# Kernel optimization log

Measured on AMD Instinct MI355X. Metric: run time of the kernel, lower is better.

Reference implementation:

```python
import jax, jax.numpy as jnp
import numpy as np

NUM_FEATURES = 128
NUM_FILTERS = 128

def setup_inputs() -> dict:
    key = jax.random.key(0)
    k1, k2, k3, k4, k5 = jax.random.split(key, 5)
    B, N, F = 4, 2048, NUM_FEATURES
    x = jax.random.normal(k1, (B, N, F), dtype=jnp.float32)
    A = jax.random.normal(k2, (B, N, N), dtype=jnp.float32)
    # Conv1D(num_filters, kernel_size=1, use_bias=False) == per-node linear F -> filters
    W = jax.random.normal(k3, (F, NUM_FILTERS), dtype=jnp.float32) * (1.0 / np.sqrt(F))
    # self.a: Conv1D(1, kernel_size=1) with bias == linear filters -> 1 (shared for x_i and x_j)
    a_w = jax.random.normal(k4, (NUM_FILTERS, 1), dtype=jnp.float32) * (1.0 / np.sqrt(NUM_FILTERS))
    a_b = jax.random.normal(k5, (1,), dtype=jnp.float32) * 0.01
    bias = jnp.zeros((NUM_FILTERS,), dtype=jnp.float32)
    return {"x": x, "A": A, "W": W, "a_w": a_w, "a_b": a_b, "bias": bias}

def reference(x, A, W, a_w, a_b, bias):
    # project features: [B,N,F] @ [F,Ff] -> [B,N,Ff]
    h = jnp.einsum('bnf,fg->bng', x, W)
    # shared attention projection (x_i and x_j use the same layer): [B,N,1]
    s = jnp.einsum('bng,go->bno', h, a_w) + a_b
    # additive scores s_i + s_j^T -> [B,N,N]
    e = s + jnp.swapaxes(s, 1, 2)
    e = jnp.where(e >= 0, e, 0.2 * e)  # LeakyReLU(0.2)
    attn = jax.nn.softmax(e + A, axis=-1)
    out = jnp.einsum('bij,bjg->big', attn, h) + bias
    return out
```

## Files before the change

kernel.cpp:

```cpp
#include <hip/hip_runtime.h>
#include <hip/hip_bf16.h>
#include <stdint.h>

#define BB 4
#define NN 2048
#define FF 128

typedef __attribute__((ext_vector_type(8))) short bf16x8;
typedef __attribute__((ext_vector_type(4))) float f32x4;

__device__ inline unsigned pk_bf16(float a, float b) {
    union { float f; unsigned u; } x, y;
    x.f = a; y.f = b;
    unsigned xu = x.u + (0x7fffu + ((x.u >> 16) & 1u));
    unsigned yu = y.u + (0x7fffu + ((y.u >> 16) & 1u));
    return (xu >> 16) | (yu & 0xffff0000u);
}

#define XT_P 136
#define WT_P 136

__global__ __launch_bounds__(256) void k1_proj(
    const float* __restrict__ x, const float* __restrict__ W,
    const float* __restrict__ a_w, const float* __restrict__ a_b,
    uint16_t* __restrict__ Ht, float* __restrict__ s_out)
{
    __shared__ uint16_t xt[16 * XT_P];
    __shared__ uint16_t Wt[128 * WT_P];
    __shared__ float sredw[4 * 16];

    const int t = threadIdx.x;
    const int w = t >> 6, l = t & 63;
    const int m16 = l & 15, q = l >> 4;
    const int b = blockIdx.x >> 7;
    const int n0 = (blockIdx.x & 127) << 4;

    const int c4 = (t & 31) * 4, kh = (t >> 5) * 16;
    float4 wr0[8], wr1[8];
    #pragma unroll
    for (int kk = 0; kk < 8; ++kk) {
        const int k = kh + 2 * kk;
        wr0[kk] = *(const float4*)(W + (size_t)k * 128 + c4);
        wr1[kk] = *(const float4*)(W + (size_t)(k + 1) * 128 + c4);
    }
    {
        const int row = t >> 4, c0 = (t & 15) * 8;
        const float* xr = x + ((size_t)(b * NN + n0 + row)) * FF + c0;
        const float4 v0 = *(const float4*)xr;
        const float4 v1 = *(const float4*)(xr + 4);
        unsigned* dst = (unsigned*)(xt + row * XT_P + c0);
        dst[0] = pk_bf16(v0.x, v0.y); dst[1] = pk_bf16(v0.z, v0.w);
        dst[2] = pk_bf16(v1.x, v1.y); dst[3] = pk_bf16(v1.z, v1.w);
    }
    #pragma unroll
    for (int kk = 0; kk < 8; ++kk) {
        const int k = kh + 2 * kk;
        *(unsigned*)(Wt + (c4 + 0) * WT_P + k) = pk_bf16(wr0[kk].x, wr1[kk].x);
        *(unsigned*)(Wt + (c4 + 1) * WT_P + k) = pk_bf16(wr0[kk].y, wr1[kk].y);
        *(unsigned*)(Wt + (c4 + 2) * WT_P + k) = pk_bf16(wr0[kk].z, wr1[kk].z);
        *(unsigned*)(Wt + (c4 + 3) * WT_P + k) = pk_bf16(wr0[kk].w, wr1[kk].w);
    }
    const int g0 = (2 * w) * 16 + m16, g1 = (2 * w + 1) * 16 + m16;
    const float aw0 = a_w[g0], aw1 = a_w[g1];
    __syncthreads();

    f32x4 acc0 = {}, acc1 = {};
    bf16x8 af[4];
    #pragma unroll
    for (int dk = 0; dk < 4; ++dk)
        af[dk] = *(const bf16x8*)(xt + m16 * XT_P + dk * 32 + q * 8);
    #pragma unroll
    for (int dk = 0; dk < 4; ++dk) {
        bf16x8 b0 = *(const bf16x8*)(Wt + g0 * WT_P + dk * 32 + q * 8);
        bf16x8 b1 = *(const bf16x8*)(Wt + g1 * WT_P + dk * 32 + q * 8);
        acc0 = __builtin_amdgcn_mfma_f32_16x16x32_bf16(af[dk], b0, acc0, 0, 0, 0);
        acc1 = __builtin_amdgcn_mfma_f32_16x16x32_bf16(af[dk], b1, acc1, 0, 0, 0);
    }

    float sp[4];
    #pragma unroll
    for (int r = 0; r < 4; ++r) sp[r] = acc0[r] * aw0 + acc1[r] * aw1;
    #pragma unroll
    for (int off = 1; off < 16; off <<= 1)
        #pragma unroll
        for (int r = 0; r < 4; ++r) sp[r] += __shfl_xor(sp[r], off, 64);
    if (m16 == 0) {
        #pragma unroll
        for (int r = 0; r < 4; ++r) sredw[w * 16 + q * 4 + r] = sp[r];
    }
    {
        uint2 o0 = { pk_bf16(acc0[0], acc0[1]), pk_bf16(acc0[2], acc0[3]) };
        uint2 o1 = { pk_bf16(acc1[0], acc1[1]), pk_bf16(acc1[2], acc1[3]) };
        *(uint2*)(Ht + ((size_t)(b * 128 + g0)) * NN + n0 + q * 4) = o0;
        *(uint2*)(Ht + ((size_t)(b * 128 + g1)) * NN + n0 + q * 4) = o1;
    }
    __syncthreads();
    if (t < 16)
        s_out[b * NN + n0 + t] = sredw[t] + sredw[16 + t] + sredw[32 + t] + sredw[48 + t] + a_b[0];
}

#define JS 8
#define IRND 8

__global__ __launch_bounds__(256, 2) void k2_attn(
    const float* __restrict__ A, const uint16_t* __restrict__ Ht,
    const float* __restrict__ s, uint16_t* __restrict__ po,
    float* __restrict__ prs)
{
    __shared__ float Opw[4][16 * 132];
    __shared__ float rsw[4][16];

    const int t = threadIdx.x;
    const int w = t >> 6, l = t & 63;
    const int m16 = l & 15, q = l >> 4;

    const int bx = blockIdx.x;
    const int js = bx & 7;
    const int is = (bx >> 3) & 15;
    const int b  = bx >> 7;
    const int j0 = js * 256;
    const int ibase = is * 128;

    const float* sb = s + b * NN;
    const float* Ab = A + (size_t)b * NN * NN;
    const uint16_t* Hb = Ht + (size_t)b * FF * NN;

    const int jc0 = j0 + w * 32 + q * 8;
    const int jc1 = j0 + (w + 4) * 32 + q * 8;

    float4 sj00 = *(const float4*)(sb + jc0);
    float4 sj01 = *(const float4*)(sb + jc0 + 4);
    float4 sj10 = *(const float4*)(sb + jc1);
    float4 sj11 = *(const float4*)(sb + jc1 + 4);

    bf16x8 hf0[8], hf1[8];
    #pragma unroll
    for (int gt = 0; gt < 8; ++gt) {
        const uint16_t* hp = Hb + (size_t)(gt * 16 + m16) * NN;
        hf0[gt] = *(const bf16x8*)(hp + jc0);
        hf1[gt] = *(const bf16x8*)(hp + jc1);
    }

    const float* Ar0 = Ab + (size_t)(ibase + m16) * NN;
    const float* Ar1 = Ab + (size_t)(ibase + 16 + m16) * NN;
    float4 p000 = *(const float4*)(Ar0 + jc0);
    float4 p001 = *(const float4*)(Ar0 + jc0 + 4);
    float4 p010 = *(const float4*)(Ar0 + jc1);
    float4 p011 = *(const float4*)(Ar0 + jc1 + 4);
    float4 p100 = *(const float4*)(Ar1 + jc0);
    float4 p101 = *(const float4*)(Ar1 + jc0 + 4);
    float4 p110 = *(const float4*)(Ar1 + jc1);
    float4 p111 = *(const float4*)(Ar1 + jc1 + 4);
    float si0 = sb[ibase + m16];
    float si1 = sb[ibase + 16 + m16];

    const size_t slice = (size_t)(js * BB + b);

    #pragma unroll
    for (int r = 0; r < IRND; ++r) {
        const int i0r = ibase + r * 16;
        const int i2  = ibase + ((r + 2) & (IRND - 1)) * 16;

        const float* An = Ab + (size_t)(i2 + m16) * NN;
        float4 n00 = *(const float4*)(An + jc0);
        float4 n01 = *(const float4*)(An + jc0 + 4);
        float4 n10 = *(const float4*)(An + jc1);
        float4 n11 = *(const float4*)(An + jc1 + 4);
        const float si2 = sb[i2 + m16];

        const float svv[16] = {sj00.x,sj00.y,sj00.z,sj00.w, sj01.x,sj01.y,sj01.z,sj01.w,
                               sj10.x,sj10.y,sj10.z,sj10.w, sj11.x,sj11.y,sj11.z,sj11.w};
        const float avv[16] = {p000.x,p000.y,p000.z,p000.w, p001.x,p001.y,p001.z,p001.w,
                               p010.x,p010.y,p010.z,p010.w, p011.x,p011.y,p011.z,p011.w};
        float pv[16]; float rs = 0.f;
        #pragma unroll
        for (int j = 0; j < 16; ++j) {
            float e = si0 + svv[j];
            e = fmaxf(e, 0.2f * e);
            pv[j] = __expf(e + avv[j]);
            rs += pv[j];
        }
        union { unsigned u[4]; bf16x8 v; } fa0, fa1;
        #pragma unroll
        for (int j = 0; j < 4; ++j) {
            fa0.u[j] = pk_bf16(pv[2 * j], pv[2 * j + 1]);
            fa1.u[j] = pk_bf16(pv[8 + 2 * j], pv[9 + 2 * j]);
        }

        f32x4 acc[8];
        #pragma unroll
        for (int gt = 0; gt < 8; ++gt) {
            f32x4 z = {0.f, 0.f, 0.f, 0.f};
            z = __builtin_amdgcn_mfma_f32_16x16x32_bf16(fa0.v, hf0[gt], z, 0, 0, 0);
            acc[gt] = __builtin_amdgcn_mfma_f32_16x16x32_bf16(fa1.v, hf1[gt], z, 0, 0, 0);
        }

        rs += __shfl_xor(rs, 16, 64);
        rs += __shfl_xor(rs, 32, 64);
        if (q == 0) rsw[w][m16] = rs;

        #pragma unroll
        for (int gt = 0; gt < 8; ++gt)
            #pragma unroll
            for (int rr = 0; rr < 4; ++rr)
                Opw[w][(q * 4 + rr) * 132 + gt * 16 + m16] = acc[gt][rr];
        asm volatile("s_waitcnt lgkmcnt(0)\n\ts_barrier" ::: "memory");

        {
            const int row = t >> 4, k8 = (t & 15) * 8;
            float v[8] = {0.f,0.f,0.f,0.f,0.f,0.f,0.f,0.f};
            #pragma unroll
            for (int sl = 0; sl < 4; ++sl) {
                float4 u0 = *(const float4*)&Opw[sl][row * 132 + k8];
                float4 u1 = *(const float4*)&Opw[sl][row * 132 + k8 + 4];
                v[0] += u0.x; v[1] += u0.y; v[2] += u0.z; v[3] += u0.w;
                v[4] += u1.x; v[5] += u1.y; v[6] += u1.z; v[7] += u1.w;
            }
            unsigned* op = (unsigned*)(po + ((slice * NN + i0r + row) * FF + k8));
            op[0] = pk_bf16(v[0], v[1]); op[1] = pk_bf16(v[2], v[3]);
            op[2] = pk_bf16(v[4], v[5]); op[3] = pk_bf16(v[6], v[7]);
            if (t < 16)
                prs[slice * NN + i0r + t] = rsw[0][t] + rsw[1][t] + rsw[2][t] + rsw[3][t];
        }
        asm volatile("s_waitcnt lgkmcnt(0)\n\ts_barrier" ::: "memory");

        p000 = p100; p001 = p101; p010 = p110; p011 = p111; si0 = si1;
        p100 = n00;  p101 = n01;  p110 = n10;  p111 = n11;  si1 = si2;
    }
}

__global__ __launch_bounds__(256) void k3_red(
    const uint16_t* __restrict__ po, const float* __restrict__ prs,
    const float* __restrict__ bias, float* __restrict__ out)
{
    const int gid = blockIdx.x * 256 + threadIdx.x;
    const int g8 = (gid & 15) * 8;
    const int i = (gid >> 4) & (NN - 1);
    const int b = gid >> 15;

    float v[8] = {0.f,0.f,0.f,0.f,0.f,0.f,0.f,0.f};
    float rsum = 0.f;
    #pragma unroll
    for (int js = 0; js < JS; ++js) {
        const size_t base = (size_t)(js * BB + b) * NN + i;
        const uint4 pv_ = *(const uint4*)(po + base * FF + g8);
        const unsigned uu[4] = {pv_.x, pv_.y, pv_.z, pv_.w};
        #pragma unroll
        for (int k = 0; k < 4; ++k) {
            union { unsigned u; float f; } lo, hi;
            lo.u = uu[k] << 16;
            hi.u = uu[k] & 0xffff0000u;
            v[2 * k]     += lo.f;
            v[2 * k + 1] += hi.f;
        }
        rsum += prs[base];
    }
    const float inv = 1.0f / rsum;
    const float4 b0 = *(const float4*)(bias + g8);
    const float4 b1 = *(const float4*)(bias + g8 + 4);
    float4 o0 = { v[0]*inv + b0.x, v[1]*inv + b0.y, v[2]*inv + b0.z, v[3]*inv + b0.w };
    float4 o1 = { v[4]*inv + b1.x, v[5]*inv + b1.y, v[6]*inv + b1.z, v[7]*inv + b1.w };
    float* op = out + ((size_t)(b * NN + i)) * FF + g8;
    *(float4*)op = o0;
    *(float4*)(op + 4) = o1;
}

extern "C" void kernel_launch(void* const* d_in, const int* in_sizes, int n_in,
                              void* d_out, int out_size, void* d_ws, size_t ws_size,
                              hipStream_t stream) {
    const float* x    = (const float*)d_in[0];
    const float* A    = (const float*)d_in[1];
    const float* W    = (const float*)d_in[2];
    const float* a_w  = (const float*)d_in[3];
    const float* a_b  = (const float*)d_in[4];
    const float* bias = (const float*)d_in[5];
    float* out = (float*)d_out;

    char* ws = (char*)d_ws;
    uint16_t* Ht = (uint16_t*)ws;
    float* s = (float*)(ws + 2 * 1024 * 1024);
    uint16_t* po = (uint16_t*)(ws + 2 * 1024 * 1024 + 65536);
    float* prs = (float*)(ws + 2 * 1024 * 1024 + 65536 + (size_t)JS * BB * NN * FF * 2);

    k1_proj<<<BB * (NN / 16), 256, 0, stream>>>(x, W, a_w, a_b, Ht, s);
    k2_attn<<<JS * 16 * BB, 256, 0, stream>>>(A, Ht, s, po, prs);
    k3_red<<<(BB * NN * FF) / (256 * 8), 256, 0, stream>>>(po, prs, bias, out);
}
```

Measured before the change: 122.7 us.

## Stage A tiles into LDS via direct global-to-LDS loads with double buffering

```diff
diff --git a/kernel.cpp b/kernel.cpp
--- a/kernel.cpp
+++ b/kernel.cpp
@@ -15,6 +15,13 @@
     unsigned xu = x.u + (0x7fffu + ((x.u >> 16) & 1u));
     unsigned yu = y.u + (0x7fffu + ((y.u >> 16) & 1u));
     return (xu >> 16) | (yu & 0xffff0000u);
+}
+
+__device__ inline void gload_lds16(const float* g, float* l) {
+    __builtin_amdgcn_global_load_lds(
+        (const __attribute__((address_space(1))) unsigned*)(g),
+        (__attribute__((address_space(3))) unsigned*)(l),
+        16, 0, 0);
 }
 
 #define XT_P 136
@@ -107,6 +114,7 @@
     const float* __restrict__ s, uint16_t* __restrict__ po,
     float* __restrict__ prs)
 {
+    __shared__ float Abuf[2][16 * 256];
     __shared__ float Opw[4][16 * 132];
     __shared__ float rsw[4][16];
 
@@ -115,9 +123,9 @@
     const int m16 = l & 15, q = l >> 4;
 
     const int bx = blockIdx.x;
-    const int js = bx & 7;
-    const int is = (bx >> 3) & 15;
-    const int b  = bx >> 7;
+    const int b  = bx & 3;
+    const int js = (bx >> 2) & 7;
+    const int is = bx >> 5;
     const int j0 = js * 256;
     const int ibase = is * 128;
 
@@ -141,37 +149,49 @@
         hf1[gt] = *(const bf16x8*)(hp + jc1);
     }
 
-    const float* Ar0 = Ab + (size_t)(ibase + m16) * NN;
-    const float* Ar1 = Ab + (size_t)(ibase + 16 + m16) * NN;
-    float4 p000 = *(const float4*)(Ar0 + jc0);
-    float4 p001 = *(const float4*)(Ar0 + jc0 + 4);
-    float4 p010 = *(const float4*)(Ar0 + jc1);
-    float4 p011 = *(const float4*)(Ar0 + jc1 + 4);
-    float4 p100 = *(const float4*)(Ar1 + jc0);
-    float4 p101 = *(const float4*)(Ar1 + jc0 + 4);
-    float4 p110 = *(const float4*)(Ar1 + jc1);
-    float4 p111 = *(const float4*)(Ar1 + jc1 + 4);
-    float si0 = sb[ibase + m16];
-    float si1 = sb[ibase + 16 + m16];
+    float si_all[IRND];
+    #pragma unroll
+    for (int rr = 0; rr < IRND; ++rr) si_all[rr] = sb[ibase + rr * 16 + m16];
+
+    #pragma unroll
+    for (int k = 0; k < 4; ++k) {
+        const int row = (w << 2) + k;
+        const float* gp = Ab + (size_t)(ibase + row) * NN + j0 + ((l ^ (row & 7)) << 2);
+        gload_lds16(gp, &Abuf[0][row * 256]);
+    }
+    asm volatile("s_waitcnt vmcnt(0)" ::: "memory");
+    __syncthreads();
 
     const size_t slice = (size_t)(js * BB + b);
+    const int s8x = m16 & 7;
+    const int bc = (w << 3) + (q << 1);
 
     #pragma unroll
     for (int r = 0; r < IRND; ++r) {
         const int i0r = ibase + r * 16;
-        const int i2  = ibase + ((r + 2) & (IRND - 1)) * 16;
-
-        const float* An = Ab + (size_t)(i2 + m16) * NN;
-        float4 n00 = *(const float4*)(An + jc0);
-        float4 n01 = *(const float4*)(An + jc0 + 4);
-        float4 n10 = *(const float4*)(An + jc1);
-        float4 n11 = *(const float4*)(An + jc1 + 4);
-        const float si2 = sb[i2 + m16];
+        const int cur = r & 1;
+
+        if (r < IRND - 1) {
+            #pragma unroll
+            for (int k = 0; k < 4; ++k) {
+                const int row = (w << 2) + k;
+                const float* gp = Ab + (size_t)(i0r + 16 + row) * NN + j0
+                                + ((l ^ (row & 7)) << 2);
+                gload_lds16(gp, &Abuf[cur ^ 1][row * 256]);
+            }
+        }
+
+        const float* Al = Abuf[cur] + m16 * 256;
+        const float4 a00 = *(const float4*)(Al + (((bc)      ^ s8x) << 2));
+        const float4 a01 = *(const float4*)(Al + (((bc + 1)  ^ s8x) << 2));
+        const float4 a10 = *(const float4*)(Al + (((bc + 32) ^ s8x) << 2));
+        const float4 a11 = *(const float4*)(Al + (((bc + 33) ^ s8x) << 2));
 
         const float svv[16] = {sj00.x,sj00.y,sj00.z,sj00.w, sj01.x,sj01.y,sj01.z,sj01.w,
                                sj10.x,sj10.y,sj10.z,sj10.w, sj11.x,sj11.y,sj11.z,sj11.w};
-        const float avv[16] = {p000.x,p000.y,p000.z,p000.w, p001.x,p001.y,p001.z,p001.w,
-                               p010.x,p010.y,p010.z,p010.w, p011.x,p011.y,p011.z,p011.w};
+        const float avv[16] = {a00.x,a00.y,a00.z,a00.w, a01.x,a01.y,a01.z,a01.w,
+                               a10.x,a10.y,a10.z,a10.w, a11.x,a11.y,a11.z,a11.w};
+        const float si0 = si_all[r];
         float pv[16]; float rs = 0.f;
         #pragma unroll
         for (int j = 0; j < 16; ++j) {
@@ -216,6 +236,7 @@
                 v[0] += u0.x; v[1] += u0.y; v[2] += u0.z; v[3] += u0.w;
                 v[4] += u1.x; v[5] += u1.y; v[6] += u1.z; v[7] += u1.w;
             }
+            asm volatile("s_waitcnt vmcnt(0)" ::: "memory");
             unsigned* op = (unsigned*)(po + ((slice * NN + i0r + row) * FF + k8));
             op[0] = pk_bf16(v[0], v[1]); op[1] = pk_bf16(v[2], v[3]);
             op[2] = pk_bf16(v[4], v[5]); op[3] = pk_bf16(v[6], v[7]);
@@ -223,9 +244,6 @@
                 prs[slice * NN + i0r + t] = rsw[0][t] + rsw[1][t] + rsw[2][t] + rsw[3][t];
         }
         asm volatile("s_waitcnt lgkmcnt(0)\n\ts_barrier" ::: "memory");
-
-        p000 = p100; p001 = p101; p010 = p110; p011 = p111; si0 = si1;
-        p100 = n00;  p101 = n01;  p110 = n10;  p111 = n11;  si1 = si2;
     }
 }
 
```

After: 124.0 us. Within noise of the previous version (+1.0%).
